# Optimization experiments

Hardware: AMD Instinct MI355X
Metric: run time of the kernel (lower is better)

Reference implementation:

```python
import jax, jax.numpy as jnp
import numpy as np

D_MODEL = 1024
N_HEAD = 16
B, S = 2, 2048


def setup_inputs() -> dict:
    key = jax.random.key(0)
    ks = jax.random.split(key, 12)
    scale = 1.0 / np.sqrt(D_MODEL)
    inp = {
        "q": jax.random.normal(ks[0], (B, S, D_MODEL), jnp.float32),
        "k": jax.random.normal(ks[1], (B, S, D_MODEL), jnp.float32),
        "v": jax.random.normal(ks[2], (B, S, D_MODEL), jnp.float32),
        "mask": jax.random.randint(ks[3], (B, S, S), 0, 2, jnp.int32),
        "Wq": jax.random.normal(ks[4], (D_MODEL, D_MODEL), jnp.float32) * scale,
        "bq": jnp.zeros((D_MODEL,), jnp.float32),
        "Wk": jax.random.normal(ks[5], (D_MODEL, D_MODEL), jnp.float32) * scale,
        "bk": jnp.zeros((D_MODEL,), jnp.float32),
        "Wv": jax.random.normal(ks[6], (D_MODEL, D_MODEL), jnp.float32) * scale,
        "bv": jnp.zeros((D_MODEL,), jnp.float32),
        "Wo": jax.random.normal(ks[7], (D_MODEL, D_MODEL), jnp.float32) * scale,
        "bo": jnp.zeros((D_MODEL,), jnp.float32),
    }
    return inp


def reference(q, k, v, mask, Wq, bq, Wk, bk, Wv, bv, Wo, bo):
    b, s, d = q.shape
    dh = d // N_HEAD

    def proj_split(x, W, bias):
        # torch nn.Linear: x @ W.T + b; then split to [b, h, s, dh]
        y = x @ W.T + bias
        return y.reshape(b, s, N_HEAD, dh).transpose(0, 2, 1, 3)

    qh = proj_split(q, Wq, bq)
    kh = proj_split(k, Wk, bk)
    vh = proj_split(v, Wv, bv)

    # score: [b, h, s_q, s_k]
    score = jnp.einsum("bhqd,bhkd->bhqk", qh, kh) / jnp.sqrt(jnp.float32(dh))
    score = jnp.where(mask[:, None, :, :] == 0, jnp.float32(-10000.0), score)
    attn = jax.nn.softmax(score, axis=-1)

    out = jnp.einsum("bhqk,bhkd->bhqd", attn, vh)
    out = out.transpose(0, 2, 1, 3).reshape(b, s, d)
    return out @ Wo.T + bo
```

## Files before the change

kernel.cpp:

```cpp
#include <hip/hip_runtime.h>

typedef unsigned short u16;
typedef __bf16 bf16x8 __attribute__((ext_vector_type(8)));
typedef float f32x4 __attribute__((ext_vector_type(4)));

#define D_MODEL 1024
#define NH 16
#define DH 64
#define BB 2
#define SS 2048

__device__ __forceinline__ u16 f2bf_fast(float f) {
    union { float f; unsigned int u; } v; v.f = f;
    return (u16)((v.u + 0x8000u) >> 16);
}
__device__ __forceinline__ uint4 pack8(const float4& a, const float4& b) {
    unsigned int a0 = __float_as_uint(a.x) + 0x8000u, a1 = __float_as_uint(a.y) + 0x8000u;
    unsigned int a2 = __float_as_uint(a.z) + 0x8000u, a3 = __float_as_uint(a.w) + 0x8000u;
    unsigned int b0 = __float_as_uint(b.x) + 0x8000u, b1 = __float_as_uint(b.y) + 0x8000u;
    unsigned int b2 = __float_as_uint(b.z) + 0x8000u, b3 = __float_as_uint(b.w) + 0x8000u;
    uint4 r;
    r.x = __builtin_amdgcn_perm(a1, a0, 0x07060302);
    r.y = __builtin_amdgcn_perm(a3, a2, 0x07060302);
    r.z = __builtin_amdgcn_perm(b1, b0, 0x07060302);
    r.w = __builtin_amdgcn_perm(b3, b2, 0x07060302);
    return r;
}

__device__ __forceinline__ void gld16(const void* g, void* l) {
    __builtin_amdgcn_global_load_lds(
        (const __attribute__((address_space(1))) unsigned int*)g,
        (__attribute__((address_space(3))) unsigned int*)l, 16, 0, 0);
}

__global__ __launch_bounds__(256) void cvtw_kernel(
    const float* __restrict__ Wq, const float* __restrict__ Wk,
    const float* __restrict__ Wv, const float* __restrict__ Wo, u16* __restrict__ cW)
{
    int z = blockIdx.y;
    const float* src = (z == 0) ? Wq : (z == 1) ? Wk : (z == 2) ? Wv : Wo;
    u16* dst = cW + (size_t)z * D_MODEL * D_MODEL;
    size_t base = ((size_t)blockIdx.x * 256 + threadIdx.x) * 8;
    float4 a = *reinterpret_cast<const float4*>(src + base);
    float4 b = *reinterpret_cast<const float4*>(src + base + 4);
    *reinterpret_cast<uint4*>(dst + base) = pack8(a, b);
}

__global__ __launch_bounds__(256) void cvtin_kernel(
    const float* __restrict__ q, const float* __restrict__ k,
    const float* __restrict__ v, u16* __restrict__ qb)
{
    int z = blockIdx.y;
    const float* src = (z == 0) ? q : (z == 1) ? k : v;
    u16* dst = qb + (size_t)z * BB * SS * D_MODEL;
    size_t base = ((size_t)blockIdx.x * 256 + threadIdx.x) * 8;
    float4 a = *reinterpret_cast<const float4*>(src + base);
    float4 b = *reinterpret_cast<const float4*>(src + base + 4);
    *reinterpret_cast<uint4*>(dst + base) = pack8(a, b);
}

__global__ __launch_bounds__(256) void maskpack_kernel(
    const int* __restrict__ mask, unsigned long long* __restrict__ pm)
{
    int gw = (blockIdx.x * 256 + threadIdx.x) >> 6;
    int l = threadIdx.x & 63;
#pragma unroll 4
    for (int i = 0; i < 32; ++i) {
        int widx = gw * 32 + i;
        int m = mask[(size_t)widx * 64 + l];
        unsigned long long bits = __ballot(m != 0);
        if (l == 0) pm[widx] = bits;
    }
}

template<int OF32, int QKV>
__device__ void gemm_bb(const u16* __restrict__ A, const u16* __restrict__ W,
                        const float* __restrict__ bias, void* outp, float oscale)
{
    __shared__ __align__(16) u16 smem[128 * 144];
    u16* lA = smem;
    u16* lW = smem + 128 * 64;
    const int t = threadIdx.x, w = t >> 6, l = t & 63;
    const int blockM = blockIdx.x * 128, blockN = blockIdx.y * 128;
    const int lrow = l >> 3, lcol = (l & 7) * 8;
    const int quad = l >> 4, c16 = l & 15;

    f32x4 acc[4][4] = {};

    for (int kt = 0; kt < 16; ++kt) {
        __syncthreads();
#pragma unroll
        for (int i = 0; i < 4; ++i) {
            int c = w * 4 + i;
            int row = c * 8 + lrow;
            gld16(A + (size_t)(blockM + row) * 1024 + kt * 64 + lcol, &lA[c * 512]);
            gld16(W + (size_t)(blockN + row) * 1024 + kt * 64 + lcol, &lW[c * 512]);
        }
        __syncthreads();
#pragma unroll
        for (int ks = 0; ks < 2; ++ks) {
            bf16x8 af[4], bfr[4];
#pragma unroll
            for (int mi = 0; mi < 4; ++mi)
                af[mi] = *reinterpret_cast<const bf16x8*>(
                    &lA[((w & 1) * 64 + mi * 16 + c16) * 64 + ks * 32 + quad * 8]);
#pragma unroll
            for (int ni = 0; ni < 4; ++ni)
                bfr[ni] = *reinterpret_cast<const bf16x8*>(
                    &lW[((w >> 1) * 64 + ni * 16 + c16) * 64 + ks * 32 + quad * 8]);
#pragma unroll
            for (int mi = 0; mi < 4; ++mi)
#pragma unroll
                for (int ni = 0; ni < 4; ++ni)
                    acc[mi][ni] = __builtin_amdgcn_mfma_f32_16x16x32_bf16(
                        af[mi], bfr[ni], acc[mi][ni], 0, 0, 0);
        }
    }

    if (QKV) {
        __syncthreads();
        const int m_base = (w & 1) * 64, n_base = (w >> 1) * 64;
#pragma unroll
        for (int ni = 0; ni < 4; ++ni) {
            int n_local = n_base + ni * 16 + c16;
            float bv = bias[blockN + n_local];
#pragma unroll
            for (int mi = 0; mi < 4; ++mi)
#pragma unroll
                for (int r = 0; r < 4; ++r) {
                    int m_local = m_base + mi * 16 + quad * 4 + r;
                    smem[m_local * 136 + n_local] =
                        f2bf_fast((acc[mi][ni][r] + bv) * oscale);
                }
        }
        __syncthreads();
        const int bb = blockM >> 11, s_base = blockM & 2047;
        u16* outb = (u16*)outp;
#pragma unroll
        for (int i = 0; i < 8; ++i) {
            int idx = t + i * 256;
            int mrow = idx >> 4, ch = idx & 15;
            uint4 val = *reinterpret_cast<const uint4*>(&smem[mrow * 136 + ch * 8]);
            int gn = blockN + ch * 8;
            int hh = gn >> 6, dh = gn & 63;
            *reinterpret_cast<uint4*>(
                outb + (((size_t)(bb * NH + hh)) * SS + s_base + mrow) * DH + dh) = val;
        }
        return;
    }

    const int m0 = blockM + (w & 1) * 64, n0 = blockN + (w >> 1) * 64;
#pragma unroll
    for (int ni = 0; ni < 4; ++ni) {
        int n = n0 + ni * 16 + c16;
        float bv = bias[n];
#pragma unroll
        for (int mi = 0; mi < 4; ++mi) {
#pragma unroll
            for (int r = 0; r < 4; ++r) {
                int m = m0 + mi * 16 + quad * 4 + r;
                float val = (acc[mi][ni][r] + bv) * oscale;
                ((float*)outp)[(size_t)m * 1024 + n] = val;
            }
        }
    }
}

__global__ __launch_bounds__(256) void qkv_kernel(
    const u16* __restrict__ qb, const u16* __restrict__ cW,
    const float* __restrict__ bq, const float* __restrict__ bk, const float* __restrict__ bv,
    u16* __restrict__ qh, u16* __restrict__ kh, u16* __restrict__ vh)
{
    int z = blockIdx.z;
    const u16* A = qb + (size_t)z * BB * SS * D_MODEL;
    const u16* W = cW + (size_t)z * D_MODEL * D_MODEL;
    const float* bias = (z == 0) ? bq : (z == 1) ? bk : bv;
    u16* out = (z == 0) ? qh : (z == 1) ? kh : vh;
    float oscale = (z == 0) ? 0.125f : 1.0f;
    gemm_bb<0, 1>(A, W, bias, out, oscale);
}

__global__ __launch_bounds__(256) void oproj_kernel(
    const u16* __restrict__ A, const u16* __restrict__ cWo,
    const float* __restrict__ bo, float* __restrict__ out)
{
    gemm_bb<1, 0>(A, cWo, bo, out, 1.0f);
}

__global__ __launch_bounds__(256) void attn_kernel(
    const u16* __restrict__ qh, const u16* __restrict__ kh, const u16* __restrict__ vh,
    const unsigned long long* __restrict__ pm, u16* __restrict__ ao)
{
    __shared__ __align__(16) u16 lQ[64 * 72];
    __shared__ __align__(16) u16 lK[64 * 72];
    __shared__ __align__(16) u16 lVt[64 * 72];
    __shared__ __align__(16) u16 lP[64 * 72];

    const int t = threadIdx.x, w = t >> 6, l = t & 63;
    const int qt = blockIdx.x, h = blockIdx.y, b = blockIdx.z;
    const int sq0 = qt * 64;
    const size_t headbase = ((size_t)(b * NH + h)) * SS * DH;
    const int quad = l >> 4, c16 = l & 15;
    const int lrow = l >> 3, lcol = (l & 7) * 8;
    const int vd2 = t & 31, vg = t >> 5;

#pragma unroll
    for (int i = 0; i < 2; ++i) {
        int row = (w * 2 + i) * 8 + lrow;
        uint4 rq = *reinterpret_cast<const uint4*>(
            qh + headbase + (size_t)(sq0 + row) * DH + lcol);
        *reinterpret_cast<uint4*>(&lQ[row * 72 + lcol]) = rq;
    }
    __syncthreads();
    bf16x8 qf[2];
#pragma unroll
    for (int ks = 0; ks < 2; ++ks)
        qf[ks] = *reinterpret_cast<const bf16x8*>(
            &lQ[(w * 16 + c16) * 72 + ks * 32 + quad * 8]);

    f32x4 oAcc[4] = {};
    float rsumAcc = 0.f;
    const size_t pmrow = ((size_t)b * SS + sq0 + w * 16 + c16) * 32;

    uint4 rk[2];
    unsigned int rvv[8];
    unsigned long long mw_cur, mw_next;
#pragma unroll
    for (int i = 0; i < 2; ++i) {
        int row = (w * 2 + i) * 8 + lrow;
        rk[i] = *reinterpret_cast<const uint4*>(kh + headbase + (size_t)row * DH + lcol);
    }
#pragma unroll
    for (int e = 0; e < 8; ++e)
        rvv[e] = *reinterpret_cast<const unsigned int*>(
            vh + headbase + (size_t)(vg * 8 + e) * DH + vd2 * 2);
    mw_cur = pm[pmrow + 0];

    for (int kt = 0; kt < 32; ++kt) {
        __syncthreads();
#pragma unroll
        for (int i = 0; i < 2; ++i) {
            int row = (w * 2 + i) * 8 + lrow;
            *reinterpret_cast<uint4*>(&lK[row * 72 + lcol]) = rk[i];
        }
        {
            uint4 cA, cB;
            cA.x = __builtin_amdgcn_perm(rvv[1], rvv[0], 0x05040100);
            cA.y = __builtin_amdgcn_perm(rvv[3], rvv[2], 0x05040100);
            cA.z = __builtin_amdgcn_perm(rvv[5], rvv[4], 0x05040100);
            cA.w = __builtin_amdgcn_perm(rvv[7], rvv[6], 0x05040100);
            cB.x = __builtin_amdgcn_perm(rvv[1], rvv[0], 0x07060302);
            cB.y = __builtin_amdgcn_perm(rvv[3], rvv[2], 0x07060302);
            cB.z = __builtin_amdgcn_perm(rvv[5], rvv[4], 0x07060302);
            cB.w = __builtin_amdgcn_perm(rvv[7], rvv[6], 0x07060302);
            *reinterpret_cast<uint4*>(&lVt[(2 * vd2) * 72 + vg * 8]) = cA;
            *reinterpret_cast<uint4*>(&lVt[(2 * vd2 + 1) * 72 + vg * 8]) = cB;
        }
        __syncthreads();
        {
            int ktn = (kt < 31) ? kt + 1 : kt;
            const int sk0n = ktn * 64;
#pragma unroll
            for (int i = 0; i < 2; ++i) {
                int row = (w * 2 + i) * 8 + lrow;
                rk[i] = *reinterpret_cast<const uint4*>(
                    kh + headbase + (size_t)(sk0n + row) * DH + lcol);
            }
#pragma unroll
            for (int e = 0; e < 8; ++e)
                rvv[e] = *reinterpret_cast<const unsigned int*>(
                    vh + headbase + (size_t)(sk0n + vg * 8 + e) * DH + vd2 * 2);
            mw_next = pm[pmrow + ktn];
        }

        f32x4 sAcc[4] = {};
#pragma unroll
        for (int ks = 0; ks < 2; ++ks) {
#pragma unroll
            for (int ni = 0; ni < 4; ++ni) {
                bf16x8 kf = *reinterpret_cast<const bf16x8*>(
                    &lK[(ni * 16 + c16) * 72 + ks * 32 + quad * 8]);
                sAcc[ni] = __builtin_amdgcn_mfma_f32_16x16x32_bf16(
                    kf, qf[ks], sAcc[ni], 0, 0, 0);
            }
        }

        unsigned long long mq = mw_cur >> (quad * 4);
        unsigned int mlo = (unsigned int)mq, mhi = (unsigned int)(mq >> 32);
#pragma unroll
        for (int ni = 0; ni < 4; ++ni) {
            unsigned int half = (ni < 2) ? mlo : mhi;
            unsigned int sh = (ni & 1) * 16;
            unsigned int w0, w1;
            {
                float p0 = ((half >> (sh + 0)) & 1u) ? __expf(sAcc[ni][0]) : 0.f;
                float p1 = ((half >> (sh + 1)) & 1u) ? __expf(sAcc[ni][1]) : 0.f;
                float p2 = ((half >> (sh + 2)) & 1u) ? __expf(sAcc[ni][2]) : 0.f;
                float p3 = ((half >> (sh + 3)) & 1u) ? __expf(sAcc[ni][3]) : 0.f;
                rsumAcc += (p0 + p1) + (p2 + p3);
                w0 = __builtin_amdgcn_perm(__float_as_uint(p1) + 0x8000u,
                                           __float_as_uint(p0) + 0x8000u, 0x07060302);
                w1 = __builtin_amdgcn_perm(__float_as_uint(p3) + 0x8000u,
                                           __float_as_uint(p2) + 0x8000u, 0x07060302);
            }
            uint2 pv; pv.x = w0; pv.y = w1;
            *reinterpret_cast<uint2*>(
                &lP[(w * 16 + c16) * 72 + ni * 16 + quad * 4]) = pv;
        }
        mw_cur = mw_next;
        __asm__ volatile("s_waitcnt lgkmcnt(0)" ::: "memory");

#pragma unroll
        for (int ks = 0; ks < 2; ++ks) {
            bf16x8 pf = *reinterpret_cast<const bf16x8*>(
                &lP[(w * 16 + c16) * 72 + ks * 32 + quad * 8]);
#pragma unroll
            for (int no = 0; no < 4; ++no) {
                bf16x8 vf = *reinterpret_cast<const bf16x8*>(
                    &lVt[(no * 16 + c16) * 72 + ks * 32 + quad * 8]);
                oAcc[no] = __builtin_amdgcn_mfma_f32_16x16x32_bf16(
                    pf, vf, oAcc[no], 0, 0, 0);
            }
        }
    }

    __syncthreads();
    float s = rsumAcc;
    s += __shfl_xor(s, 16);
    s += __shfl_xor(s, 32);
    float rinv = 1.0f / s;
    float linv[4];
#pragma unroll
    for (int r = 0; r < 4; ++r)
        linv[r] = __shfl(rinv, quad * 4 + r);
#pragma unroll
    for (int no = 0; no < 4; ++no)
#pragma unroll
        for (int r = 0; r < 4; ++r)
            lK[(w * 16 + quad * 4 + r) * 72 + no * 16 + c16] =
                f2bf_fast(oAcc[no][r] * linv[r]);
    __syncthreads();
#pragma unroll
    for (int i = 0; i < 2; ++i) {
        int idx = t + i * 256;
        int row = idx >> 3, ch = idx & 7;
        uint4 val = *reinterpret_cast<const uint4*>(&lK[row * 72 + ch * 8]);
        *reinterpret_cast<uint4*>(
            ao + ((size_t)b * SS + sq0 + row) * D_MODEL + h * DH + ch * 8) = val;
    }
}

extern "C" void kernel_launch(void* const* d_in, const int* in_sizes, int n_in,
                              void* d_out, int out_size, void* d_ws, size_t ws_size,
                              hipStream_t stream)
{
    const float* q    = (const float*)d_in[0];
    const float* k    = (const float*)d_in[1];
    const float* v    = (const float*)d_in[2];
    const int*   mask = (const int*)d_in[3];
    const float* Wq   = (const float*)d_in[4];
    const float* bq   = (const float*)d_in[5];
    const float* Wk   = (const float*)d_in[6];
    const float* bk   = (const float*)d_in[7];
    const float* Wv   = (const float*)d_in[8];
    const float* bv   = (const float*)d_in[9];
    const float* Wo   = (const float*)d_in[10];
    const float* bo   = (const float*)d_in[11];

    const size_t T4M = (size_t)BB * SS * D_MODEL;
    u16* qh = (u16*)d_ws;
    u16* kh = qh + T4M;
    u16* vh = kh + T4M;
    u16* ao = vh + T4M;
    u16* cW = ao + T4M;
    u16* qb = cW + 4 * (size_t)D_MODEL * D_MODEL;
    unsigned long long* pm = (unsigned long long*)(qb + 3 * T4M);
    float* out = (float*)d_out;

    cvtw_kernel<<<dim3(512, 4), 256, 0, stream>>>(Wq, Wk, Wv, Wo, cW);
    cvtin_kernel<<<dim3(2048, 3), 256, 0, stream>>>(q, k, v, qb);
    maskpack_kernel<<<1024, 256, 0, stream>>>(mask, pm);
    qkv_kernel<<<dim3(32, 8, 3), 256, 0, stream>>>(qb, cW, bq, bk, bv, qh, kh, vh);
    attn_kernel<<<dim3(32, NH, BB), 256, 0, stream>>>(qh, kh, vh, pm, ao);
    oproj_kernel<<<dim3(32, 8), 256, 0, stream>>>(ao, cW + 3 * (size_t)D_MODEL * D_MODEL, bo, out);
}
```

Baseline: 334.5 us.

## Process 128 query rows per attention block and use exp2 with prescaled Q

Each attention block now handles 128 query rows, two 16-row groups per wave, so every K/V tile staged in LDS feeds twice as many MFMAs and half as many blocks reload K/V. The Q scale folds in log2(e) so the softmax can use the hardware exp2 instead of expf. MFMA sections are wrapped in s_setprio, and launch bounds request two blocks per CU. The costs are more registers per thread and fewer blocks in the grid.

Result: faster. 303.7 us (-9.2%).

```diff
diff --git a/kernel.cpp b/kernel.cpp
--- a/kernel.cpp
+++ b/kernel.cpp
@@ -9,6 +9,12 @@
 #define DH 64
 #define BB 2
 #define SS 2048
+
+#if __has_builtin(__builtin_amdgcn_exp2f)
+#define EXP2f(x) __builtin_amdgcn_exp2f(x)
+#else
+#define EXP2f(x) exp2f(x)
+#endif
 
 __device__ __forceinline__ u16 f2bf_fast(float f) {
     union { float f; unsigned int u; } v; v.f = f;
@@ -176,7 +182,7 @@
     const u16* W = cW + (size_t)z * D_MODEL * D_MODEL;
     const float* bias = (z == 0) ? bq : (z == 1) ? bk : bv;
     u16* out = (z == 0) ? qh : (z == 1) ? kh : vh;
-    float oscale = (z == 0) ? 0.125f : 1.0f;
+    float oscale = (z == 0) ? 0.18033688011112042f : 1.0f;
     gemm_bb<0, 1>(A, W, bias, out, oscale);
 }
 
@@ -187,44 +193,46 @@
     gemm_bb<1, 0>(A, cWo, bo, out, 1.0f);
 }
 
-__global__ __launch_bounds__(256) void attn_kernel(
+__global__ __launch_bounds__(256, 2) void attn_kernel(
     const u16* __restrict__ qh, const u16* __restrict__ kh, const u16* __restrict__ vh,
     const unsigned long long* __restrict__ pm, u16* __restrict__ ao)
 {
-    __shared__ __align__(16) u16 lQ[64 * 72];
     __shared__ __align__(16) u16 lK[64 * 72];
     __shared__ __align__(16) u16 lVt[64 * 72];
-    __shared__ __align__(16) u16 lP[64 * 72];
+    __shared__ __align__(16) u16 lP[128 * 72];
 
     const int t = threadIdx.x, w = t >> 6, l = t & 63;
     const int qt = blockIdx.x, h = blockIdx.y, b = blockIdx.z;
-    const int sq0 = qt * 64;
+    const int sq0 = qt * 128;
     const size_t headbase = ((size_t)(b * NH + h)) * SS * DH;
     const int quad = l >> 4, c16 = l & 15;
     const int lrow = l >> 3, lcol = (l & 7) * 8;
     const int vd2 = t & 31, vg = t >> 5;
 
 #pragma unroll
-    for (int i = 0; i < 2; ++i) {
-        int row = (w * 2 + i) * 8 + lrow;
+    for (int i = 0; i < 4; ++i) {
+        int row = (w * 4 + i) * 8 + lrow;
         uint4 rq = *reinterpret_cast<const uint4*>(
             qh + headbase + (size_t)(sq0 + row) * DH + lcol);
-        *reinterpret_cast<uint4*>(&lQ[row * 72 + lcol]) = rq;
-    }
-    __syncthreads();
-    bf16x8 qf[2];
-#pragma unroll
-    for (int ks = 0; ks < 2; ++ks)
-        qf[ks] = *reinterpret_cast<const bf16x8*>(
-            &lQ[(w * 16 + c16) * 72 + ks * 32 + quad * 8]);
-
-    f32x4 oAcc[4] = {};
-    float rsumAcc = 0.f;
-    const size_t pmrow = ((size_t)b * SS + sq0 + w * 16 + c16) * 32;
+        *reinterpret_cast<uint4*>(&lP[row * 72 + lcol]) = rq;
+    }
+    __asm__ volatile("s_waitcnt lgkmcnt(0)" ::: "memory");
+    bf16x8 qf[2][2];
+#pragma unroll
+    for (int g = 0; g < 2; ++g)
+#pragma unroll
+        for (int ks = 0; ks < 2; ++ks)
+            qf[g][ks] = *reinterpret_cast<const bf16x8*>(
+                &lP[(w * 32 + g * 16 + c16) * 72 + ks * 32 + quad * 8]);
+
+    f32x4 oAcc[2][4] = {};
+    float rsumAcc[2] = {0.f, 0.f};
+    const size_t pmrow0 = ((size_t)b * SS + sq0 + w * 32 + c16) * 32;
+    const size_t pmrow1 = pmrow0 + 16 * 32;
 
     uint4 rk[2];
     unsigned int rvv[8];
-    unsigned long long mw_cur, mw_next;
+    unsigned long long mw_cur0, mw_cur1, mw_next0, mw_next1;
 #pragma unroll
     for (int i = 0; i < 2; ++i) {
         int row = (w * 2 + i) * 8 + lrow;
@@ -234,7 +242,8 @@
     for (int e = 0; e < 8; ++e)
         rvv[e] = *reinterpret_cast<const unsigned int*>(
             vh + headbase + (size_t)(vg * 8 + e) * DH + vd2 * 2);
-    mw_cur = pm[pmrow + 0];
+    mw_cur0 = pm[pmrow0 + 0];
+    mw_cur1 = pm[pmrow1 + 0];
 
     for (int kt = 0; kt < 32; ++kt) {
         __syncthreads();
@@ -270,81 +279,102 @@
             for (int e = 0; e < 8; ++e)
                 rvv[e] = *reinterpret_cast<const unsigned int*>(
                     vh + headbase + (size_t)(sk0n + vg * 8 + e) * DH + vd2 * 2);
-            mw_next = pm[pmrow + ktn];
-        }
-
-        f32x4 sAcc[4] = {};
+            mw_next0 = pm[pmrow0 + ktn];
+            mw_next1 = pm[pmrow1 + ktn];
+        }
+
+        f32x4 sAcc[2][4] = {};
+        __builtin_amdgcn_s_setprio(1);
 #pragma unroll
         for (int ks = 0; ks < 2; ++ks) {
 #pragma unroll
             for (int ni = 0; ni < 4; ++ni) {
                 bf16x8 kf = *reinterpret_cast<const bf16x8*>(
                     &lK[(ni * 16 + c16) * 72 + ks * 32 + quad * 8]);
-                sAcc[ni] = __builtin_amdgcn_mfma_f32_16x16x32_bf16(
-                    kf, qf[ks], sAcc[ni], 0, 0, 0);
+                sAcc[0][ni] = __builtin_amdgcn_mfma_f32_16x16x32_bf16(
+                    kf, qf[0][ks], sAcc[0][ni], 0, 0, 0);
+                sAcc[1][ni] = __builtin_amdgcn_mfma_f32_16x16x32_bf16(
+                    kf, qf[1][ks], sAcc[1][ni], 0, 0, 0);
             }
         }
-
-        unsigned long long mq = mw_cur >> (quad * 4);
-        unsigned int mlo = (unsigned int)mq, mhi = (unsigned int)(mq >> 32);
-#pragma unroll
-        for (int ni = 0; ni < 4; ++ni) {
-            unsigned int half = (ni < 2) ? mlo : mhi;
-            unsigned int sh = (ni & 1) * 16;
-            unsigned int w0, w1;
-            {
-                float p0 = ((half >> (sh + 0)) & 1u) ? __expf(sAcc[ni][0]) : 0.f;
-                float p1 = ((half >> (sh + 1)) & 1u) ? __expf(sAcc[ni][1]) : 0.f;
-                float p2 = ((half >> (sh + 2)) & 1u) ? __expf(sAcc[ni][2]) : 0.f;
-                float p3 = ((half >> (sh + 3)) & 1u) ? __expf(sAcc[ni][3]) : 0.f;
-                rsumAcc += (p0 + p1) + (p2 + p3);
-                w0 = __builtin_amdgcn_perm(__float_as_uint(p1) + 0x8000u,
-                                           __float_as_uint(p0) + 0x8000u, 0x07060302);
-                w1 = __builtin_amdgcn_perm(__float_as_uint(p3) + 0x8000u,
-                                           __float_as_uint(p2) + 0x8000u, 0x07060302);
+        __builtin_amdgcn_s_setprio(0);
+
+#pragma unroll
+        for (int g = 0; g < 2; ++g) {
+            unsigned long long mw = g ? mw_cur1 : mw_cur0;
+            unsigned long long mq = mw >> (quad * 4);
+            unsigned int mlo = (unsigned int)mq, mhi = (unsigned int)(mq >> 32);
+            float rs = 0.f;
+#pragma unroll
+            for (int ni = 0; ni < 4; ++ni) {
+                unsigned int half = (ni < 2) ? mlo : mhi;
+                unsigned int sh = (ni & 1) * 16;
+                unsigned int w0, w1;
+                {
+                    float p0 = ((half >> (sh + 0)) & 1u) ? EXP2f(sAcc[g][ni][0]) : 0.f;
+                    float p1 = ((half >> (sh + 1)) & 1u) ? EXP2f(sAcc[g][ni][1]) : 0.f;
+                    float p2 = ((half >> (sh + 2)) & 1u) ? EXP2f(sAcc[g][ni][2]) : 0.f;
+                    float p3 = ((half >> (sh + 3)) & 1u) ? EXP2f(sAcc[g][ni][3]) : 0.f;
+                    rs += (p0 + p1) + (p2 + p3);
+                    w0 = __builtin_amdgcn_perm(__float_as_uint(p1) + 0x8000u,
+                                               __float_as_uint(p0) + 0x8000u, 0x07060302);
+                    w1 = __builtin_amdgcn_perm(__float_as_uint(p3) + 0x8000u,
+                                               __float_as_uint(p2) + 0x8000u, 0x07060302);
+                }
+                uint2 pv; pv.x = w0; pv.y = w1;
+                *reinterpret_cast<uint2*>(
+                    &lP[(w * 32 + g * 16 + c16) * 72 + ni * 16 + quad * 4]) = pv;
             }
-            uint2 pv; pv.x = w0; pv.y = w1;
-            *reinterpret_cast<uint2*>(
-                &lP[(w * 16 + c16) * 72 + ni * 16 + quad * 4]) = pv;
-        }
-        mw_cur = mw_next;
+            if (g == 0) rsumAcc[0] += rs; else rsumAcc[1] += rs;
+        }
+        mw_cur0 = mw_next0; mw_cur1 = mw_next1;
         __asm__ volatile("s_waitcnt lgkmcnt(0)" ::: "memory");
 
+        __builtin_amdgcn_s_setprio(1);
 #pragma unroll
         for (int ks = 0; ks < 2; ++ks) {
-            bf16x8 pf = *reinterpret_cast<const bf16x8*>(
-                &lP[(w * 16 + c16) * 72 + ks * 32 + quad * 8]);
+            bf16x8 pf0 = *reinterpret_cast<const bf16x8*>(
+                &lP[(w * 32 + c16) * 72 + ks * 32 + quad * 8]);
+            bf16x8 pf1 = *reinterpret_cast<const bf16x8*>(
+                &lP[(w * 32 + 16 + c16) * 72 + ks * 32 + quad * 8]);
 #pragma unroll
             for (int no = 0; no < 4; ++no) {
                 bf16x8 vf = *reinterpret_cast<const bf16x8*>(
                     &lVt[(no * 16 + c16) * 72 + ks * 32 + quad * 8]);
-                oAcc[no] = __builtin_amdgcn_mfma_f32_16x16x32_bf16(
-                    pf, vf, oAcc[no], 0, 0, 0);
+                oAcc[0][no] = __builtin_amdgcn_mfma_f32_16x16x32_bf16(
+                    pf0, vf, oAcc[0][no], 0, 0, 0);
+                oAcc[1][no] = __builtin_amdgcn_mfma_f32_16x16x32_bf16(
+                    pf1, vf, oAcc[1][no], 0, 0, 0);
             }
         }
-    }
-
+        __builtin_amdgcn_s_setprio(0);
+    }
+
+    float linv[2][4];
+#pragma unroll
+    for (int g = 0; g < 2; ++g) {
+        float s = (g == 0) ? rsumAcc[0] : rsumAcc[1];
+        s += __shfl_xor(s, 16);
+        s += __shfl_xor(s, 32);
+        float rinv = 1.0f / s;
+#pragma unroll
+        for (int r = 0; r < 4; ++r)
+            linv[g][r] = __shfl(rinv, quad * 4 + r);
+    }
+#pragma unroll
+    for (int g = 0; g < 2; ++g)
+#pragma unroll
+        for (int no = 0; no < 4; ++no)
+#pragma unroll
+            for (int r = 0; r < 4; ++r)
+                lP[(w * 32 + g * 16 + quad * 4 + r) * 72 + no * 16 + c16] =
+                    f2bf_fast(oAcc[g][no][r] * linv[g][r]);
     __syncthreads();
-    float s = rsumAcc;
-    s += __shfl_xor(s, 16);
-    s += __shfl_xor(s, 32);
-    float rinv = 1.0f / s;
-    float linv[4];
-#pragma unroll
-    for (int r = 0; r < 4; ++r)
-        linv[r] = __shfl(rinv, quad * 4 + r);
-#pragma unroll
-    for (int no = 0; no < 4; ++no)
-#pragma unroll
-        for (int r = 0; r < 4; ++r)
-            lK[(w * 16 + quad * 4 + r) * 72 + no * 16 + c16] =
-                f2bf_fast(oAcc[no][r] * linv[r]);
-    __syncthreads();
-#pragma unroll
-    for (int i = 0; i < 2; ++i) {
+#pragma unroll
+    for (int i = 0; i < 4; ++i) {
         int idx = t + i * 256;
         int row = idx >> 3, ch = idx & 7;
-        uint4 val = *reinterpret_cast<const uint4*>(&lK[row * 72 + ch * 8]);
+        uint4 val = *reinterpret_cast<const uint4*>(&lP[row * 72 + ch * 8]);
         *reinterpret_cast<uint4*>(
             ao + ((size_t)b * SS + sq0 + row) * D_MODEL + h * DH + ch * 8) = val;
     }
@@ -381,6 +411,6 @@
     cvtin_kernel<<<dim3(2048, 3), 256, 0, stream>>>(q, k, v, qb);
     maskpack_kernel<<<1024, 256, 0, stream>>>(mask, pm);
     qkv_kernel<<<dim3(32, 8, 3), 256, 0, stream>>>(qb, cW, bq, bk, bv, qh, kh, vh);
-    attn_kernel<<<dim3(32, NH, BB), 256, 0, stream>>>(qh, kh, vh, pm, ao);
+    attn_kernel<<<dim3(16, NH, BB), 256, 0, stream>>>(qh, kh, vh, pm, ao);
     oproj_kernel<<<dim3(32, 8), 256, 0, stream>>>(ao, cW + 3 * (size_t)D_MODEL * D_MODEL, bo, out);
 }
```
